# Optimization experiments

Measured on AMD Instinct MI355X. Metric: run time of the kernel, lower is better.

Reference implementation:

```python
import jax, jax.numpy as jnp
import numpy as np

Q = 1024      # query length
R = 2048      # relative position length (2*Q, mems=None)
B = 2         # batch
D_MODEL = 1024
N_HEAD = 16
D_HEAD = 64
SCALE = 1.0 / (D_HEAD ** 0.5)
LN_EPS = 1e-12


def setup_inputs() -> dict:
    key = jax.random.key(0)
    ks = jax.random.split(key, 16)
    f32 = jnp.float32
    n = lambda k, s, sc=1.0: jax.random.normal(k, s, f32) * sc
    return {
        "h": n(ks[0], (Q, B, D_MODEL)),
        "r": n(ks[1], (R, B, D_MODEL)),
        "seg_mat": jax.random.randint(ks[2], (Q, Q, B), 0, 2).astype(bool),
        "attn_mask": jax.random.randint(ks[3], (Q, Q, B, 1), 0, 2).astype(f32),
        "q_kernel": n(ks[4], (D_MODEL, N_HEAD, D_HEAD), 0.02),
        "k_kernel": n(ks[5], (D_MODEL, N_HEAD, D_HEAD), 0.02),
        "v_kernel": n(ks[6], (D_MODEL, N_HEAD, D_HEAD), 0.02),
        "r_kernel": n(ks[7], (D_MODEL, N_HEAD, D_HEAD), 0.02),
        "o_kernel": n(ks[8], (D_MODEL, N_HEAD, D_HEAD), 0.02),
        "r_w_bias": n(ks[9], (N_HEAD, D_HEAD), 0.02),
        "r_r_bias": n(ks[10], (N_HEAD, D_HEAD), 0.02),
        "r_s_bias": n(ks[11], (N_HEAD, D_HEAD), 0.02),
        "seg_embed": n(ks[12], (2, N_HEAD, D_HEAD), 0.02),
        "ln_gamma": jnp.ones((D_MODEL,), f32),
        "ln_beta": jnp.zeros((D_MODEL,), f32),
    }


def _rel_shift(x, klen):
    # x: [q, rlen, b, n] -> [q, klen, b, n]
    q, rlen, b, n = x.shape
    x = x.reshape(rlen, q, b, n)[1:]
    x = x.reshape(q, rlen - 1, b, n)[:, :klen]
    return x


def _layer_norm(x, gamma, beta):
    mu = jnp.mean(x, axis=-1, keepdims=True)
    var = jnp.mean(jnp.square(x - mu), axis=-1, keepdims=True)
    return (x - mu) * jax.lax.rsqrt(var + LN_EPS) * gamma + beta


def reference(h, r, seg_mat, attn_mask, q_kernel, k_kernel, v_kernel,
              r_kernel, o_kernel, r_w_bias, r_r_bias, r_s_bias, seg_embed,
              ln_gamma, ln_beta):
    # projections (mems=None -> cat == h)
    q_head = jnp.einsum('ibh,hnd->ibnd', h, q_kernel)
    k_head = jnp.einsum('ibh,hnd->ibnd', h, k_kernel)
    v_head = jnp.einsum('ibh,hnd->ibnd', h, v_kernel)
    k_head_r = jnp.einsum('ibh,hnd->ibnd', r, r_kernel)

    klen = k_head.shape[0]
    # content score
    ac = jnp.einsum('ibnd,jbnd->ijbn', q_head + r_w_bias, k_head)
    # relative-position score with rel_shift
    bd = jnp.einsum('ibnd,jbnd->ijbn', q_head + r_r_bias, k_head_r)
    bd = _rel_shift(bd, klen)
    # segment bias: ef [q, 2, b, n] -> select per (i,j,b) via seg_mat
    ef = jnp.einsum('ibnd,snd->isbn', q_head + r_s_bias, seg_embed)
    ef = jnp.where(seg_mat[:, :, :, None], ef[:, 1:, :, :], ef[:, :1, :, :])

    attn_score = (ac + bd + ef) * SCALE
    attn_score = attn_score - 1e30 * attn_mask
    attn_prob = jax.nn.softmax(attn_score, axis=1)  # over key axis j

    attn_vec = jnp.einsum('ijbn,jbnd->ibnd', attn_prob, v_head)
    output = jnp.einsum('ibnd,hnd->ibh', attn_vec, o_kernel)
    return _layer_norm(output + h, ln_gamma, ln_beta)
```

## Files before the change

kernel.cpp:

```cpp
#include <hip/hip_runtime.h>

typedef __bf16 bf16x8 __attribute__((ext_vector_type(8)));
typedef float f32x4 __attribute__((ext_vector_type(4)));
typedef unsigned short us4 __attribute__((ext_vector_type(4)));

__device__ __forceinline__ unsigned short f2bf(float f) {
  unsigned int u = __builtin_bit_cast(unsigned int, f);
  u += 0x7fffu + ((u >> 16) & 1u);
  return (unsigned short)(u >> 16);
}
__device__ __forceinline__ float bf2f(unsigned short s) {
  unsigned int u = ((unsigned int)s) << 16;
  return __builtin_bit_cast(float, u);
}
__device__ __forceinline__ f32x4 mfma16(bf16x8 a, bf16x8 b, f32x4 c) {
  return __builtin_amdgcn_mfma_f32_16x16x32_bf16(a, b, c, 0, 0, 0);
}
__device__ __forceinline__ void gload16(const void* g, void* l) {
  __builtin_amdgcn_global_load_lds(
      (const __attribute__((address_space(1))) unsigned int*)g,
      (__attribute__((address_space(3))) unsigned int*)l, 16, 0, 0);
}
__device__ __forceinline__ float fexp2(float x) {
  float r;
  asm("v_exp_f32 %0, %1" : "=v"(r) : "v"(x));
  return r;
}
template <int CTRL>
__device__ __forceinline__ float dppf(float x) {
  return __builtin_bit_cast(
      float, __builtin_amdgcn_mov_dpp(__builtin_bit_cast(int, x), CTRL, 0xf, 0xf, true));
}
__device__ __forceinline__ float rmax16(float x) {
  x = fmaxf(x, dppf<0xB1>(x));
  x = fmaxf(x, dppf<0x4E>(x));
  x = fmaxf(x, dppf<0x124>(x));
  x = fmaxf(x, dppf<0x128>(x));
  return x;
}
__device__ __forceinline__ float rsum16(float x) {
  x += dppf<0xB1>(x);
  x += dppf<0x4E>(x);
  x += dppf<0x124>(x);
  x += dppf<0x128>(x);
  return x;
}

#define QSCL 0.18033688011112042f
#define LOG2E 1.4426950408889634f

__global__ __launch_bounds__(256) void pre_kernel(
    const float* __restrict__ h, const float* __restrict__ r, const float* __restrict__ wo,
    const float* __restrict__ w0, const float* __restrict__ w1,
    const float* __restrict__ w2, const float* __restrict__ w3,
    const unsigned char* __restrict__ seg, const float* __restrict__ mask,
    unsigned short* __restrict__ hb, unsigned short* __restrict__ rb,
    unsigned short* __restrict__ wo_b,
    unsigned short* __restrict__ o0, unsigned short* __restrict__ o1,
    unsigned short* __restrict__ o2, unsigned short* __restrict__ o3,
    unsigned int* __restrict__ segout) {
  __shared__ float t[32][33];
  const int bx = blockIdx.x;
  const int tid = threadIdx.x;
  if (bx < 7168) {
    int idx = bx * 256 + tid;
    const float* in;
    unsigned short* out;
    int o;
    if (idx < 524288) { in = h; out = hb; o = idx; }
    else if (idx < 1572864) { in = r; out = rb; o = idx - 524288; }
    else { in = wo; out = wo_b; o = idx - 1572864; }
    float4 v = ((const float4*)in)[o];
    us4 tt;
    tt[0] = f2bf(v.x); tt[1] = f2bf(v.y); tt[2] = f2bf(v.z); tt[3] = f2bf(v.w);
    *(us4*)&out[o * 4] = tt;
  } else if (bx < 11264) {
    int zz = bx - 7168;
    int z = zz >> 10, tt_ = zz & 1023;
    const float* in = z == 0 ? w0 : (z == 1 ? w1 : (z == 2 ? w2 : w3));
    unsigned short* out = z == 0 ? o0 : (z == 1 ? o1 : (z == 2 ? o2 : o3));
    int k0 = (tt_ >> 5) * 32;
    int n0 = (tt_ & 31) * 32;
    int rr = tid >> 5;
    int c = tid & 31;
#pragma unroll
    for (int s = 0; s < 4; ++s)
      t[rr + s * 8][c] = in[(k0 + rr + s * 8) * 1024 + n0 + c];
    __syncthreads();
#pragma unroll
    for (int s = 0; s < 4; ++s)
      out[(n0 + rr + s * 8) * 1024 + k0 + c] = f2bf(t[c][rr + s * 8]);
  } else {
    int ij = (bx - 11264) * 256 + tid;
    unsigned short sv = *(const unsigned short*)&seg[ij * 2];
    float2 mv = *(const float2*)&mask[(size_t)ij * 2];
    unsigned int q0 = ((unsigned int)f2bf(mv.x * -1.4426950408889634e30f) << 16) |
                      ((sv & 0xffu) ? 0x3f80u : 0u);
    unsigned int q1 = ((unsigned int)f2bf(mv.y * -1.4426950408889634e30f) << 16) |
                      ((sv >> 8) ? 0x3f80u : 0u);
    segout[ij] = q0;
    segout[1048576 + ij] = q1;
  }
}

__global__ __launch_bounds__(512) void proj4_kernel(
    const unsigned short* __restrict__ hb, const unsigned short* __restrict__ rb,
    const unsigned short* __restrict__ wq_t, const unsigned short* __restrict__ wk_t,
    const unsigned short* __restrict__ wv_t, const unsigned short* __restrict__ wr_t,
    const float* __restrict__ rwb, const float* __restrict__ rrb, const float* __restrict__ rsb,
    const float* __restrict__ seg_embed,
    unsigned short* __restrict__ qwb, unsigned short* __restrict__ qrb,
    unsigned short* __restrict__ khb, unsigned short* __restrict__ vhb,
    unsigned short* __restrict__ krhb,
    float* __restrict__ dvb) {
  __shared__ unsigned short sA[2][128 * 64];
  __shared__ unsigned short sB[2][128 * 64];
  const int bx = blockIdx.x;
  int sel, rblk;
  const unsigned short* A;
  if (bx < 384) { sel = bx >> 7; rblk = bx & 127; A = hb; }
  else { sel = 3; rblk = bx - 384; A = rb; }
  const unsigned short* Bt = sel == 0 ? wq_t : (sel == 1 ? wk_t : (sel == 2 ? wv_t : wr_t));
  const int n0 = (rblk & 7) * 128, m0 = (rblk >> 3) * 128;
  const int tid = threadIdx.x, lane = tid & 63, w = tid >> 6;
  const int wm = w >> 1, wn = w & 1, g = lane >> 4, lc = lane & 15;

  f32x4 acc[2][4] = {};

  auto STAGE = [&](int buf, int kt) {
#pragma unroll
    for (int s = 0; s < 2; ++s) {
      int c = s * 512 + tid;
      int row = c >> 3;
      int ko = ((c & 7) ^ (row & 7)) * 8;
      int lbase = (s * 512 + w * 64) * 8;
      gload16(&A[(size_t)(m0 + row) * 1024 + kt + ko], &sA[buf][lbase]);
      gload16(&Bt[(size_t)(n0 + row) * 1024 + kt + ko], &sB[buf][lbase]);
    }
  };

  STAGE(0, 0);
  __syncthreads();

  for (int kt = 0; kt < 1024; kt += 64) {
    const int cur = (kt >> 6) & 1;
    if (kt < 960) STAGE(cur ^ 1, kt + 64);
    bf16x8 af[2][2], bfr[4][2];
#pragma unroll
    for (int ks = 0; ks < 2; ++ks) {
#pragma unroll
      for (int mi = 0; mi < 2; ++mi) {
        int ra = wm * 32 + mi * 16 + lc;
        af[mi][ks] = *(const bf16x8*)&sA[cur][ra * 64 + (((ks * 4 + g) ^ (ra & 7)) * 8)];
      }
#pragma unroll
      for (int ni = 0; ni < 4; ++ni) {
        int rb_ = wn * 64 + ni * 16 + lc;
        bfr[ni][ks] = *(const bf16x8*)&sB[cur][rb_ * 64 + (((ks * 4 + g) ^ (rb_ & 7)) * 8)];
      }
    }
#pragma unroll
    for (int ks = 0; ks < 2; ++ks)
#pragma unroll
      for (int mi = 0; mi < 2; ++mi)
#pragma unroll
        for (int ni = 0; ni < 4; ++ni)
          acc[mi][ni] = mfma16(af[mi][ks], bfr[ni][ks], acc[mi][ni]);
    __syncthreads();
  }

  if (sel == 0) {
    const int hn = (n0 >> 6) + wn;
    float sedv[4], bwv[4], brv[4], bsv[4];
#pragma unroll
    for (int ni = 0; ni < 4; ++ni) {
      int col = n0 + wn * 64 + ni * 16 + lc;
      sedv[ni] = seg_embed[1024 + hn * 64 + ni * 16 + lc] - seg_embed[hn * 64 + ni * 16 + lc];
      bwv[ni] = rwb[col];
      brv[ni] = rrb[col];
      bsv[ni] = rsb[col];
    }
#pragma unroll
    for (int mi = 0; mi < 2; ++mi) {
      int rowb = m0 + wm * 32 + mi * 16 + g * 4;
#pragma unroll
      for (int r = 0; r < 4; ++r) {
        float e = 0.f;
#pragma unroll
        for (int ni = 0; ni < 4; ++ni) {
          int col = n0 + wn * 64 + ni * 16 + lc;
          float v = acc[mi][ni][r];
          size_t idx = (size_t)(rowb + r) * 1024 + col;
          qwb[idx] = f2bf((v + bwv[ni]) * QSCL);
          qrb[idx] = f2bf((v + brv[ni]) * QSCL);
          e += (v + bsv[ni]) * 0.125f * sedv[ni];
        }
        e = rsum16(e);
        if (lc == 0) {
          int ib = rowb + r;
          int i = ib >> 1, b = ib & 1;
          dvb[(b * 16 + hn) * 1024 + i] = e * LOG2E;
        }
      }
    }
  } else {
#pragma unroll
    for (int ni = 0; ni < 4; ++ni) {
      int col = n0 + wn * 64 + ni * 16 + lc;
#pragma unroll
      for (int mi = 0; mi < 2; ++mi) {
        int rowb = m0 + wm * 32 + mi * 16 + g * 4;
#pragma unroll
        for (int r = 0; r < 4; ++r) {
          float v = acc[mi][ni][r];
          size_t idx = (size_t)(rowb + r) * 1024 + col;
          if (sel == 1) khb[idx] = f2bf(v);
          else if (sel == 2) vhb[idx] = f2bf(v);
          else krhb[idx] = f2bf(v);
        }
      }
    }
  }
}

__global__ __launch_bounds__(512) void gemm64_out(const unsigned short* __restrict__ A,
                                                  const unsigned short* __restrict__ Bt,
                                                  float* __restrict__ C) {
  __shared__ unsigned short sA[2][64 * 64];
  __shared__ unsigned short sB[2][128 * 64];
  const int tid = threadIdx.x, lane = tid & 63, w = tid >> 6;
  const int wm = w >> 2, wn = w & 3, g = lane >> 4, lc = lane & 15;
  const int m0 = blockIdx.y * 64, n0 = blockIdx.x * 128;
  f32x4 acc[2][2] = {};

  auto STAGE = [&](int buf, int kt) {
    {
      int c = tid;
      int row = c >> 3;
      int ko = ((c & 7) ^ (row & 7)) * 8;
      gload16(&A[(size_t)(m0 + row) * 1024 + kt + ko], &sA[buf][w * 64 * 8]);
    }
#pragma unroll
    for (int s = 0; s < 2; ++s) {
      int c = s * 512 + tid;
      int row = c >> 3;
      int ko = ((c & 7) ^ (row & 7)) * 8;
      gload16(&Bt[(size_t)(n0 + row) * 1024 + kt + ko], &sB[buf][(s * 512 + w * 64) * 8]);
    }
  };

  STAGE(0, 0);
  __syncthreads();

  for (int kt = 0; kt < 1024; kt += 64) {
    const int cur = (kt >> 6) & 1;
    if (kt < 960) STAGE(cur ^ 1, kt + 64);
    bf16x8 af[2][2], bfr[2][2];
#pragma unroll
    for (int ks = 0; ks < 2; ++ks) {
#pragma unroll
      for (int mi = 0; mi < 2; ++mi) {
        int ra = wm * 32 + mi * 16 + lc;
        af[mi][ks] = *(const bf16x8*)&sA[cur][ra * 64 + (((ks * 4 + g) ^ (ra & 7)) * 8)];
      }
#pragma unroll
      for (int ni = 0; ni < 2; ++ni) {
        int rb_ = wn * 32 + ni * 16 + lc;
        bfr[ni][ks] = *(const bf16x8*)&sB[cur][rb_ * 64 + (((ks * 4 + g) ^ (rb_ & 7)) * 8)];
      }
    }
#pragma unroll
    for (int ks = 0; ks < 2; ++ks)
#pragma unroll
      for (int mi = 0; mi < 2; ++mi)
#pragma unroll
        for (int ni = 0; ni < 2; ++ni)
          acc[mi][ni] = mfma16(af[mi][ks], bfr[ni][ks], acc[mi][ni]);
    __syncthreads();
  }
#pragma unroll
  for (int ni = 0; ni < 2; ++ni) {
    int col = n0 + wn * 32 + ni * 16 + lc;
#pragma unroll
    for (int mi = 0; mi < 2; ++mi) {
      int rowb = m0 + wm * 32 + mi * 16 + g * 4;
#pragma unroll
      for (int r = 0; r < 4; ++r)
        C[(size_t)(rowb + r) * 1024 + col] = acc[mi][ni][r];
    }
  }
}

__global__ __launch_bounds__(256) void transpose_v(const unsigned short* __restrict__ vh,
                                                   unsigned short* __restrict__ vT) {
  __shared__ unsigned short t[64][65];
  const int bn = blockIdx.y, j0 = blockIdx.x * 64;
  const int b = bn >> 4, n = bn & 15;
  const int r = threadIdx.x >> 4;
  const int c4 = (threadIdx.x & 15) * 4;
#pragma unroll
  for (int s = 0; s < 4; ++s) {
    int j = r + s * 16;
    us4 v = *(const us4*)&vh[((size_t)(j0 + j) * 2 + b) * 1024 + n * 64 + c4];
    t[j][c4 + 0] = v[0]; t[j][c4 + 1] = v[1]; t[j][c4 + 2] = v[2]; t[j][c4 + 3] = v[3];
  }
  __syncthreads();
#pragma unroll
  for (int s = 0; s < 4; ++s) {
    int d = r + s * 16;
    us4 v;
    v[0] = t[c4 + 0][d]; v[1] = t[c4 + 1][d]; v[2] = t[c4 + 2][d]; v[3] = t[c4 + 3][d];
    *(us4*)&vT[((size_t)bn * 64 + d) * 1024 + j0 + c4] = v;
  }
}

__global__ __launch_bounds__(512, 4) void attn_kernel(
    const unsigned short* __restrict__ qw, const unsigned short* __restrict__ qr,
    const unsigned short* __restrict__ kh, const unsigned short* __restrict__ krh,
    const unsigned short* __restrict__ vT,
    const float* __restrict__ dvb,
    const unsigned int* __restrict__ segmask,
    float* __restrict__ part, float* __restrict__ ml) {
  __shared__ unsigned short sK[64][72];
  __shared__ unsigned short sVT[64][72];
  __shared__ unsigned short sKR[256][72];
  __shared__ unsigned short sP[8][16][80];

  const int tid = threadIdx.x, lane = tid & 63, w = tid >> 6;
  const int g = lane >> 4, lc = lane & 15;
  const int bn = blockIdx.x, b = bn >> 4, n = bn & 15;
  const int i0 = blockIdx.y * 128;
  const int js = blockIdx.z;
  const int S0 = 1024 + js * 512 - i0 - 127;

  bf16x8 fqw[2], fqr[2];
  const int qrow = i0 + w * 16 + lc;
#pragma unroll
  for (int ks = 0; ks < 2; ++ks) {
    size_t off = ((size_t)qrow * 2 + b) * 1024 + n * 64 + ks * 32 + g * 8;
    fqw[ks] = *(const bf16x8*)&qw[off];
    fqr[ks] = *(const bf16x8*)&qr[off];
  }
  float dv[4];
  unsigned int smoff[4];
#pragma unroll
  for (int r = 0; r < 4; ++r) {
    int i = i0 + w * 16 + g * 4 + r;
    dv[r] = dvb[bn * 1024 + i];
    smoff[r] = ((unsigned)b << 20) | ((unsigned)i << 10) | (unsigned)lc;
  }
  float mrun[4], lsum[4];
  f32x4 accO[4] = {};
#pragma unroll
  for (int r = 0; r < 4; ++r) { mrun[r] = -3e38f; lsum[r] = 0.f; }

  const int srow = tid >> 3;
  const int sko = (tid & 7) * 8;

#pragma unroll
  for (int pp = 0; pp < 3; ++pp) {
    int jr = S0 + pp * 64 + srow;
    *(uint4*)&sKR[jr & 255][sko] =
        *(const uint4*)&krh[((size_t)jr * 2 + b) * 1024 + n * 64 + sko];
  }
  int j0 = js * 512;
  uint4 rK = *(const uint4*)&kh[((size_t)(j0 + srow) * 2 + b) * 1024 + n * 64 + sko];
  uint4 rV = *(const uint4*)&vT[((size_t)bn * 64 + srow) * 1024 + j0 + sko];
  uint4 rR = *(const uint4*)&krh[((size_t)(S0 + 192 + srow) * 2 + b) * 1024 + n * 64 + sko];

  for (int t = 0; t < 8; ++t) {
    j0 = (js * 8 + t) * 64;
    __syncthreads();
    *(uint4*)&sK[srow][sko] = rK;
    *(uint4*)&sVT[srow][sko] = rV;
    if (t < 7) {
      *(uint4*)&sKR[(S0 + 192 + t * 64 + srow) & 255][sko] = rR;
      int j0n = j0 + 64;
      rK = *(const uint4*)&kh[((size_t)(j0n + srow) * 2 + b) * 1024 + n * 64 + sko];
      rV = *(const uint4*)&vT[((size_t)bn * 64 + srow) * 1024 + j0n + sko];
      if (t < 6) {
        int jr = S0 + 256 + t * 64 + srow;
        if (jr > 2047) jr = 2047;
        rR = *(const uint4*)&krh[((size_t)jr * 2 + b) * 1024 + n * 64 + sko];
      }
    }
    unsigned int msv[4][4];
#pragma unroll
    for (int r = 0; r < 4; ++r)
#pragma unroll
      for (int nf = 0; nf < 4; ++nf)
        msv[r][nf] = segmask[smoff[r] + j0 + nf * 16];
    __syncthreads();

    const int base = S0 + t * 64 + (7 - w) * 16;
    f32x4 bdk[5];
#pragma unroll
    for (int k = 0; k < 5; ++k) {
      f32x4 a = {0.f, 0.f, 0.f, 0.f};
#pragma unroll
      for (int ks = 0; ks < 2; ++ks) {
        bf16x8 fk = *(const bf16x8*)&sKR[(base + k * 16 + lc) & 255][ks * 32 + g * 8];
        a = mfma16(fqr[ks], fk, a);
      }
      bdk[k] = a;
    }
    float p[4][4];
#pragma unroll
    for (int r = 0; r < 4; ++r) {
      const int a_ = g * 4 + r;
      const int srcl = (lane & 48) | ((lc + 15 - a_) & 15);
      float s0 = __shfl(bdk[0][r], srcl);
      float s1 = __shfl(bdk[1][r], srcl);
      float s2 = __shfl(bdk[2][r], srcl);
      float s3 = __shfl(bdk[3][r], srcl);
      float s4 = __shfl(bdk[4][r], srcl);
      const bool lo = lc <= a_;
#pragma unroll
      for (int nf = 0; nf < 4; ++nf) {
        unsigned int u = msv[r][nf];
        float sgd = (u & 0xffffu) ? dv[r] : 0.f;
        float mkv = bf2f((unsigned short)(u >> 16));
        float bdv = lo ? (nf == 0 ? s0 : nf == 1 ? s1 : nf == 2 ? s2 : s3)
                       : (nf == 0 ? s1 : nf == 1 ? s2 : nf == 2 ? s3 : s4);
        p[r][nf] = sgd + mkv + bdv;
      }
    }
    f32x4 aa[4];
#pragma unroll
    for (int nf = 0; nf < 4; ++nf) {
      f32x4 a = {0.f, 0.f, 0.f, 0.f};
#pragma unroll
      for (int ks = 0; ks < 2; ++ks) {
        bf16x8 fk = *(const bf16x8*)&sK[nf * 16 + lc][ks * 32 + g * 8];
        a = mfma16(fqw[ks], fk, a);
      }
      aa[nf] = a;
    }
#pragma unroll
    for (int r = 0; r < 4; ++r)
#pragma unroll
      for (int nf = 0; nf < 4; ++nf) p[r][nf] += aa[nf][r];

#pragma unroll
    for (int r = 0; r < 4; ++r) {
      float mt = fmaxf(fmaxf(p[r][0], p[r][1]), fmaxf(p[r][2], p[r][3]));
      mt = rmax16(mt);
      float mnew = fmaxf(mrun[r], mt);
      float corr = fexp2(mrun[r] - mnew);
      mrun[r] = mnew;
      float se = 0.f;
#pragma unroll
      for (int nf = 0; nf < 4; ++nf) {
        float e = fexp2(p[r][nf] - mnew);
        p[r][nf] = e;
        se += e;
      }
      se = rsum16(se);
      lsum[r] = lsum[r] * corr + se;
#pragma unroll
      for (int df = 0; df < 4; ++df) accO[df][r] *= corr;
#pragma unroll
      for (int nf = 0; nf < 4; ++nf)
        sP[w][g * 4 + r][nf * 16 + lc] = f2bf(p[r][nf]);
    }
#pragma unroll
    for (int ks = 0; ks < 2; ++ks) {
      bf16x8 fp = *(const bf16x8*)&sP[w][lc][ks * 32 + g * 8];
#pragma unroll
      for (int df = 0; df < 4; ++df) {
        bf16x8 fv = *(const bf16x8*)&sVT[df * 16 + lc][ks * 32 + g * 8];
        accO[df] = mfma16(fp, fv, accO[df]);
      }
    }
  }
#pragma unroll
  for (int r = 0; r < 4; ++r) {
    int i = i0 + w * 16 + g * 4 + r;
    size_t pb = ((size_t)(js * 32 + bn) * 1024 + i) * 64;
#pragma unroll
    for (int df = 0; df < 4; ++df) part[pb + df * 16 + lc] = accO[df][r];
    if (lc == 0) {
      size_t mb = (((size_t)js * 32 + bn) * 1024 + i) * 2;
      ml[mb] = mrun[r];
      ml[mb + 1] = lsum[r];
    }
  }
}

__global__ __launch_bounds__(256) void combine_kernel(const float* __restrict__ part,
                                                      const float* __restrict__ ml,
                                                      unsigned short* __restrict__ av) {
  int gw = blockIdx.x * 4 + (threadIdx.x >> 6);
  int lane = threadIdx.x & 63;
  int bn = gw >> 10, i = gw & 1023;
  int b = bn >> 4, n = bn & 15;
  float m0 = ml[((size_t)bn * 1024 + i) * 2];
  float l0 = ml[((size_t)bn * 1024 + i) * 2 + 1];
  float m1 = ml[(((size_t)32 + bn) * 1024 + i) * 2];
  float l1 = ml[(((size_t)32 + bn) * 1024 + i) * 2 + 1];
  float mx = fmaxf(m0, m1);
  float w0 = fexp2(m0 - mx), w1 = fexp2(m1 - mx);
  float inv = 1.f / (l0 * w0 + l1 * w1);
  float o = part[((size_t)bn * 1024 + i) * 64 + lane] * w0 +
            part[(((size_t)32 + bn) * 1024 + i) * 64 + lane] * w1;
  av[((size_t)i * 2 + b) * 1024 + n * 64 + lane] = f2bf(o * inv);
}

__global__ __launch_bounds__(256) void ln_kernel(const float* __restrict__ gout,
                                                 const float* __restrict__ h,
                                                 const float* __restrict__ gamma,
                                                 const float* __restrict__ beta,
                                                 float* __restrict__ out) {
  __shared__ float red[8];
  const int row = blockIdx.x;
  const int tid = threadIdx.x;
  float x[4];
  float s = 0.f;
#pragma unroll
  for (int q = 0; q < 4; ++q) {
    int d = tid + q * 256;
    x[q] = gout[(size_t)row * 1024 + d] + h[(size_t)row * 1024 + d];
    s += x[q];
  }
#pragma unroll
  for (int m = 1; m < 64; m <<= 1) s += __shfl_xor(s, m);
  if ((tid & 63) == 0) red[tid >> 6] = s;
  __syncthreads();
  s = red[0] + red[1] + red[2] + red[3];
  float mu = s * (1.f / 1024.f);
  float v = 0.f;
#pragma unroll
  for (int q = 0; q < 4; ++q) {
    float dd = x[q] - mu;
    v += dd * dd;
  }
#pragma unroll
  for (int m = 1; m < 64; m <<= 1) v += __shfl_xor(v, m);
  if ((tid & 63) == 0) red[4 + (tid >> 6)] = v;
  __syncthreads();
  v = red[4] + red[5] + red[6] + red[7];
  float rstd = rsqrtf(v * (1.f / 1024.f) + 1e-12f);
#pragma unroll
  for (int q = 0; q < 4; ++q) {
    int d = tid + q * 256;
    out[(size_t)row * 1024 + d] = (x[q] - mu) * rstd * gamma[d] + beta[d];
  }
}

extern "C" void kernel_launch(void* const* d_in, const int* in_sizes, int n_in,
                              void* d_out, int out_size, void* d_ws, size_t ws_size,
                              hipStream_t stream) {
  const float* h = (const float*)d_in[0];
  const float* r = (const float*)d_in[1];
  const unsigned char* seg = (const unsigned char*)d_in[2];
  const float* mask = (const float*)d_in[3];
  const float* wq = (const float*)d_in[4];
  const float* wk = (const float*)d_in[5];
  const float* wv = (const float*)d_in[6];
  const float* wr = (const float*)d_in[7];
  const float* wo = (const float*)d_in[8];
  const float* rwb = (const float*)d_in[9];
  const float* rrb = (const float*)d_in[10];
  const float* rsb = (const float*)d_in[11];
  const float* seg_embed = (const float*)d_in[12];
  const float* gamma = (const float*)d_in[13];
  const float* beta = (const float*)d_in[14];
  float* out = (float*)d_out;

  char* ws = (char*)d_ws;
  size_t off = 0;
  auto alloc = [&](size_t bytes) {
    size_t cur = off;
    off = (off + bytes + 255) & ~(size_t)255;
    return cur;
  };
  unsigned short* hb = (unsigned short*)(ws + alloc(2048 * 1024 * 2));
  unsigned short* rb = (unsigned short*)(ws + alloc(4096 * 1024 * 2));
  unsigned short* wq_t = (unsigned short*)(ws + alloc(1024 * 1024 * 2));
  unsigned short* wk_t = (unsigned short*)(ws + alloc(1024 * 1024 * 2));
  unsigned short* wv_t = (unsigned short*)(ws + alloc(1024 * 1024 * 2));
  unsigned short* wr_t = (unsigned short*)(ws + alloc(1024 * 1024 * 2));
  unsigned short* wo_b = (unsigned short*)(ws + alloc(1024 * 1024 * 2));
  unsigned short* qwb = (unsigned short*)(ws + alloc(2048 * 1024 * 2));
  unsigned short* qrb = (unsigned short*)(ws + alloc(2048 * 1024 * 2));
  unsigned short* khb = (unsigned short*)(ws + alloc(2048 * 1024 * 2));
  unsigned short* vhb = (unsigned short*)(ws + alloc(2048 * 1024 * 2));
  unsigned short* krhb = (unsigned short*)(ws + alloc(4096 * 1024 * 2));
  unsigned short* vTb = (unsigned short*)(ws + alloc(2048 * 1024 * 2));
  float* dvb = (float*)(ws + alloc(2048 * 16 * 4));
  unsigned int* segmask = (unsigned int*)(ws + alloc(2 * 1024 * 1024 * 4));
  unsigned short* avb = (unsigned short*)(ws + alloc(2048 * 1024 * 2));
  float* gout = (float*)(ws + alloc(2048 * 1024 * 4));
  float* part = (float*)(ws + alloc((size_t)2 * 32 * 1024 * 64 * 4));
  float* mlb = (float*)(ws + alloc((size_t)2 * 32 * 1024 * 2 * 4));
  (void)ws_size; (void)in_sizes; (void)n_in; (void)out_size;

  pre_kernel<<<15360, 256, 0, stream>>>(h, r, wo, wq, wk, wv, wr, seg, mask,
                                        hb, rb, wo_b, wq_t, wk_t, wv_t, wr_t, segmask);

  proj4_kernel<<<640, 512, 0, stream>>>(hb, rb, wq_t, wk_t, wv_t, wr_t, rwb, rrb, rsb,
                                        seg_embed, qwb, qrb, khb, vhb, krhb, dvb);

  transpose_v<<<dim3(16, 32), 256, 0, stream>>>(vhb, vTb);

  attn_kernel<<<dim3(32, 8, 2), 512, 0, stream>>>(qwb, qrb, khb, krhb, vTb,
                                                  dvb, segmask, part, mlb);
  combine_kernel<<<8192, 256, 0, stream>>>(part, mlb, avb);

  gemm64_out<<<dim3(8, 32), 512, 0, stream>>>(avb, wo_b, gout);
  ln_kernel<<<2048, 256, 0, stream>>>(gout, h, gamma, beta, out);
}
```

Before: 127.9 us.

## Defer softmax rescaling, raise MFMA wave priority, store partials in bf16

The online-softmax loop now rescales the running max, sum and accumulator only when the tile max exceeds the running max by more than a threshold, which skips most correction exponentials and multiplies. MFMA sections are wrapped in s_setprio so the waves issuing matrix work are scheduled ahead of others. The split-K partial outputs are written and read as bf16 instead of fp32, which halves that traffic between attn and combine. In exchange this costs some precision, and the deferred max allows exp values up to about 2^11.5 before the accumulator is rescaled.

```diff
diff --git a/kernel.cpp b/kernel.cpp
--- a/kernel.cpp
+++ b/kernel.cpp
@@ -48,6 +48,7 @@
 
 #define QSCL 0.18033688011112042f
 #define LOG2E 1.4426950408889634f
+#define DEFER_THR 11.5f
 
 __global__ __launch_bounds__(256) void pre_kernel(
     const float* __restrict__ h, const float* __restrict__ r, const float* __restrict__ wo,
@@ -320,7 +321,7 @@
     const unsigned short* __restrict__ vT,
     const float* __restrict__ dvb,
     const unsigned int* __restrict__ segmask,
-    float* __restrict__ part, float* __restrict__ ml) {
+    unsigned short* __restrict__ part, float* __restrict__ ml) {
   __shared__ unsigned short sK[64][72];
   __shared__ unsigned short sVT[64][72];
   __shared__ unsigned short sKR[256][72];
@@ -394,6 +395,7 @@
 
     const int base = S0 + t * 64 + (7 - w) * 16;
     f32x4 bdk[5];
+    __builtin_amdgcn_s_setprio(1);
 #pragma unroll
     for (int k = 0; k < 5; ++k) {
       f32x4 a = {0.f, 0.f, 0.f, 0.f};
@@ -404,6 +406,7 @@
       }
       bdk[k] = a;
     }
+    __builtin_amdgcn_s_setprio(0);
     float p[4][4];
 #pragma unroll
     for (int r = 0; r < 4; ++r) {
@@ -426,6 +429,7 @@
       }
     }
     f32x4 aa[4];
+    __builtin_amdgcn_s_setprio(1);
 #pragma unroll
     for (int nf = 0; nf < 4; ++nf) {
       f32x4 a = {0.f, 0.f, 0.f, 0.f};
@@ -436,6 +440,7 @@
       }
       aa[nf] = a;
     }
+    __builtin_amdgcn_s_setprio(0);
 #pragma unroll
     for (int r = 0; r < 4; ++r)
 #pragma unroll
@@ -445,24 +450,27 @@
     for (int r = 0; r < 4; ++r) {
       float mt = fmaxf(fmaxf(p[r][0], p[r][1]), fmaxf(p[r][2], p[r][3]));
       mt = rmax16(mt);
-      float mnew = fmaxf(mrun[r], mt);
-      float corr = fexp2(mrun[r] - mnew);
-      mrun[r] = mnew;
+      if (mt > mrun[r] + DEFER_THR) {
+        float corr = fexp2(mrun[r] - mt);
+        mrun[r] = mt;
+        lsum[r] *= corr;
+#pragma unroll
+        for (int df = 0; df < 4; ++df) accO[df][r] *= corr;
+      }
       float se = 0.f;
 #pragma unroll
       for (int nf = 0; nf < 4; ++nf) {
-        float e = fexp2(p[r][nf] - mnew);
+        float e = fexp2(p[r][nf] - mrun[r]);
         p[r][nf] = e;
         se += e;
       }
       se = rsum16(se);
-      lsum[r] = lsum[r] * corr + se;
-#pragma unroll
-      for (int df = 0; df < 4; ++df) accO[df][r] *= corr;
+      lsum[r] += se;
 #pragma unroll
       for (int nf = 0; nf < 4; ++nf)
         sP[w][g * 4 + r][nf * 16 + lc] = f2bf(p[r][nf]);
     }
+    __builtin_amdgcn_s_setprio(1);
 #pragma unroll
     for (int ks = 0; ks < 2; ++ks) {
       bf16x8 fp = *(const bf16x8*)&sP[w][lc][ks * 32 + g * 8];
@@ -472,13 +480,14 @@
         accO[df] = mfma16(fp, fv, accO[df]);
       }
     }
+    __builtin_amdgcn_s_setprio(0);
   }
 #pragma unroll
   for (int r = 0; r < 4; ++r) {
     int i = i0 + w * 16 + g * 4 + r;
     size_t pb = ((size_t)(js * 32 + bn) * 1024 + i) * 64;
 #pragma unroll
-    for (int df = 0; df < 4; ++df) part[pb + df * 16 + lc] = accO[df][r];
+    for (int df = 0; df < 4; ++df) part[pb + df * 16 + lc] = f2bf(accO[df][r]);
     if (lc == 0) {
       size_t mb = (((size_t)js * 32 + bn) * 1024 + i) * 2;
       ml[mb] = mrun[r];
@@ -487,7 +496,7 @@
   }
 }
 
-__global__ __launch_bounds__(256) void combine_kernel(const float* __restrict__ part,
+__global__ __launch_bounds__(256) void combine_kernel(const unsigned short* __restrict__ part,
                                                       const float* __restrict__ ml,
                                                       unsigned short* __restrict__ av) {
   int gw = blockIdx.x * 4 + (threadIdx.x >> 6);
@@ -501,8 +510,8 @@
   float mx = fmaxf(m0, m1);
   float w0 = fexp2(m0 - mx), w1 = fexp2(m1 - mx);
   float inv = 1.f / (l0 * w0 + l1 * w1);
-  float o = part[((size_t)bn * 1024 + i) * 64 + lane] * w0 +
-            part[(((size_t)32 + bn) * 1024 + i) * 64 + lane] * w1;
+  float o = bf2f(part[((size_t)bn * 1024 + i) * 64 + lane]) * w0 +
+            bf2f(part[(((size_t)32 + bn) * 1024 + i) * 64 + lane]) * w1;
   av[((size_t)i * 2 + b) * 1024 + n * 64 + lane] = f2bf(o * inv);
 }
 
@@ -591,7 +600,7 @@
   unsigned int* segmask = (unsigned int*)(ws + alloc(2 * 1024 * 1024 * 4));
   unsigned short* avb = (unsigned short*)(ws + alloc(2048 * 1024 * 2));
   float* gout = (float*)(ws + alloc(2048 * 1024 * 4));
-  float* part = (float*)(ws + alloc((size_t)2 * 32 * 1024 * 64 * 4));
+  unsigned short* part = (unsigned short*)(ws + alloc((size_t)2 * 32 * 1024 * 64 * 2));
   float* mlb = (float*)(ws + alloc((size_t)2 * 32 * 1024 * 2 * 4));
   (void)ws_size; (void)in_sizes; (void)n_in; (void)out_size;
 
```

Result: slower. 172.1 us (+34.6%).
